# Kernel optimization log

Measured on AMD Instinct MI355X. Metric: run time of the kernel, lower is better.

The kernel has to match this reference:

```python
import jax, jax.numpy as jnp
import numpy as np
import math


def setup_inputs() -> dict:
    B, L, D, P, V = 4, 4096, 512, 128, 8
    key = jax.random.key(0)
    ki = iter(jax.random.split(key, 40))
    def rn(shape, s=0.02):
        return jax.random.normal(next(ki), shape, jnp.float32) * s
    z = lambda *s: jnp.zeros(s, jnp.float32)
    return dict(
        x=jax.random.normal(next(ki), (B, L, D), jnp.float32),
        W_omega=rn((D, D)), b_omega=z(D),
        omega_scale=jnp.full((D,), 0.01, jnp.float32),
        W_pi1=rn((D, D)), b_pi1=z(D), W_pi2=rn((D, D)), b_pi2=z(D),
        W_m1v=rn((D, D)), b_m1v=z(D),
        W_m1o=rn((D, D)), b_m1o=z(D),
        W_mag=rn((D, D)), b_mag=z(D),
        mag_scale=jnp.asarray(5.0, jnp.float32),
        W_qoff=rn((D, D)), b_qoff=z(D),
        W_kenc=rn((D, P)), b_kenc=z(P),
        W_venc=rn((D, V)), b_venc=z(V),
        W_sk1=rn((2 * D, D)), b_sk1=z(D),
        W_sk2=rn((D, P)), b_sk2=z(P),
        W_sg=rn((D, 1)), b_sg=z(1),
        W_kvo=rn((V, D)), b_kvo=z(D),
        ln_g=jnp.ones((4 * D,), jnp.float32), ln_b=z(4 * D),
        W_o1=rn((4 * D, 2 * D)), b_o1=z(2 * D),
        W_o2=rn((2 * D, D)), b_o2=z(D),
    )


def _lin(h, W, b):
    return h @ W + b


def _gelu(h):
    return jax.nn.gelu(h, approximate=False)  # torch nn.GELU default (erf)


def _forward(x, W_omega, b_omega, omega_scale, W_pi1, b_pi1, W_pi2, b_pi2,
             W_m1v, b_m1v, W_m1o, b_m1o, W_mag, b_mag, mag_scale,
             W_qoff, b_qoff, W_kenc, b_kenc, W_venc, b_venc,
             W_sk1, b_sk1, W_sk2, b_sk2, W_sg, b_sg, W_kvo, b_kvo,
             ln_g, ln_b, W_o1, b_o1, W_o2, b_o2):
    B, L, D = x.shape
    P = W_kenc.shape[1]
    # --- evolving phases ---
    omega_scaled = _lin(x, W_omega, b_omega) * jnp.abs(omega_scale)
    phi_init = _lin(_gelu(_lin(x, W_pi1, b_pi1)), W_pi2, b_pi2)
    phi = phi_init + jnp.cumsum(omega_scaled, axis=1)
    cos_phi, sin_phi = jnp.cos(phi), jnp.sin(phi)
    # --- memory 1: positional phasor memory ---
    v1 = _lin(x, W_m1v, b_m1v)
    magnitude = jax.nn.sigmoid(_lin(x, W_mag, b_mag)) * jnp.abs(mag_scale)
    wv1 = magnitude * v1
    sqrt_mag = jnp.sqrt(jnp.cumsum(magnitude, axis=1) + 1e-8)
    mem1_cos = jnp.cumsum(wv1 * cos_phi, axis=1) / sqrt_mag
    mem1_sin = jnp.cumsum(wv1 * sin_phi, axis=1) / sqrt_mag
    phi_q = phi + _lin(x, W_qoff, b_qoff)
    pos_ret = (mem1_cos * jnp.cos(phi_q) + mem1_sin * jnp.sin(phi_q)) / math.sqrt(D)
    pos_out = _lin(pos_ret, W_m1o, b_m1o)
    # --- memory 2: key/value phasor binding ---
    query_phase = jnp.tanh(_lin(x, W_kenc, b_kenc)) * math.pi
    values = _lin(x, W_venc, b_venc)                      # [B,L,V]
    store_gate = jax.nn.sigmoid(_lin(x, W_sg, b_sg))      # [B,L,1]
    positions = jnp.arange(1, L + 1, dtype=x.dtype)[None, :, None]
    context_avg = jnp.cumsum(x, axis=1) / positions
    sk_in = jnp.concatenate([x, context_avg], axis=-1)
    storage_phase = jnp.tanh(_lin(_gelu(_lin(sk_in, W_sk1, b_sk1)), W_sk2, b_sk2)) * math.pi
    store_cos, store_sin = jnp.cos(storage_phase), jnp.sin(storage_phase)  # [B,L,P]
    gv = values * store_gate                               # [B,L,V]
    # [B,L,P,V] outer products, cumsum along L
    kv_mem_cos = jnp.cumsum(store_cos[..., None] * gv[:, :, None, :], axis=1)
    kv_mem_sin = jnp.cumsum(store_sin[..., None] * gv[:, :, None, :], axis=1)
    gate_cum = jnp.clip(jnp.cumsum(store_gate, axis=1), 1.0, None)  # [B,L,1]
    inv_norm = (1.0 / jnp.sqrt(gate_cum))[..., None]
    kv_mem_cos = kv_mem_cos * inv_norm
    kv_mem_sin = kv_mem_sin * inv_norm
    q_cos, q_sin = jnp.cos(query_phase), jnp.sin(query_phase)
    kv_retrieved = (jnp.einsum('blp,blpv->blv', q_cos, kv_mem_cos)
                    + jnp.einsum('blp,blpv->blv', q_sin, kv_mem_sin)) / math.sqrt(P)
    kv_out = _lin(kv_retrieved, W_kvo, b_kvo)
    # --- output projection ---
    combined = jnp.concatenate([pos_out, kv_out, x * cos_phi, x * sin_phi], axis=-1)
    mu = combined.mean(axis=-1, keepdims=True)
    var = combined.var(axis=-1, keepdims=True)
    h = (combined - mu) / jnp.sqrt(var + 1e-5) * ln_g + ln_b
    h = _gelu(_lin(h, W_o1, b_o1))  # dropout is identity in eval mode
    return x + _lin(h, W_o2, b_o2)


def reference(x, W_omega, b_omega, omega_scale, W_pi1, b_pi1, W_pi2, b_pi2,
              W_m1v, b_m1v, W_m1o, b_m1o, W_mag, b_mag, mag_scale,
              W_qoff, b_qoff, W_kenc, b_kenc, W_venc, b_venc,
              W_sk1, b_sk1, W_sk2, b_sk2, W_sg, b_sg, W_kvo, b_kvo,
              ln_g, ln_b, W_o1, b_o1, W_o2, b_o2):
    return _forward(x, W_omega, b_omega, omega_scale, W_pi1, b_pi1, W_pi2, b_pi2,
                    W_m1v, b_m1v, W_m1o, b_m1o, W_mag, b_mag, mag_scale,
                    W_qoff, b_qoff, W_kenc, b_kenc, W_venc, b_venc,
                    W_sk1, b_sk1, W_sk2, b_sk2, W_sg, b_sg, W_kvo, b_kvo,
                    ln_g, ln_b, W_o1, b_o1, W_o2, b_o2)
```

## Files before the change

### kernel.cpp

```cpp
#include <hip/hip_runtime.h>
#include <math.h>

#define B_ 4
#define L_ 4096
#define D_ 512
#define P_ 128
#define V_ 8
#define N_ (B_*L_)
#define NC 64
#define CL (L_/NC)
#define LD ((size_t)L_*D_)
#define PI_F 3.14159265358979323846f

typedef unsigned short ushort;
typedef __attribute__((ext_vector_type(8))) short bh8;
typedef __attribute__((ext_vector_type(4))) float f4;
typedef const __attribute__((address_space(1))) unsigned int gu32;
typedef __attribute__((address_space(3))) unsigned int lu32;

__device__ __forceinline__ float geluf(float v){
    return 0.5f*v*(1.0f+erff(v*0.7071067811865475f));
}
__device__ __forceinline__ float tanhf_fast(float x){
    return 1.0f - 2.0f/(__expf(2.0f*x)+1.0f);
}
__device__ __forceinline__ ushort f2b(float f){
    union { float f; unsigned u; } v; v.f = f;
    unsigned r = (v.u + 0x7fffu + ((v.u >> 16) & 1u)) >> 16;
    return (ushort)r;
}
__device__ __forceinline__ float b2f(ushort h){
    union { unsigned u; float f; } v; v.u = ((unsigned)h) << 16;
    return v.f;
}
__device__ __forceinline__ void gload16(const ushort* g, ushort* l){
    __builtin_amdgcn_global_load_lds((gu32*)g, (lu32*)l, 16, 0, 0);
}
__device__ __forceinline__ int xcd_swz(int orig, int nwg){
    int q8 = nwg >> 3, r8 = nwg & 7;
    int xcd = orig & 7, sub = orig >> 3;
    return (xcd < r8 ? xcd*(q8+1) : r8*(q8+1) + (xcd-r8)*q8) + sub;
}

template<int ACT>
__global__ __launch_bounds__(512, 1)
void cgemm_k(const ushort* __restrict__ A, int lda,
             const ushort* __restrict__ Wt, const float* __restrict__ bias,
             ushort* __restrict__ Ob, float* __restrict__ Of,
             int ldc, int K, const float* __restrict__ addbuf)
{
    __shared__ ushort lA[2][256*64];
    __shared__ ushort lB[2][128*64];
    const int tid = threadIdx.x, lane = tid & 63, w = tid >> 6;
    const int wr = w >> 1, wc = w & 1;
    const int nbx = gridDim.x;
    const int wg = xcd_swz(blockIdx.y*nbx + blockIdx.x, nbx*gridDim.y);
    const int row0 = (wg / nbx) * 256, col0 = (wg % nbx) * 128;

    const int sr = tid >> 3, scp = tid & 7;
    const int scsrc = (scp ^ (sr & 7)) * 8;
    const ushort* gA = A  + (size_t)(row0 + sr) * lda + scsrc;
    const ushort* gB = Wt + (size_t)(col0 + sr) * K   + scsrc;
    const int dof = sr*64 + scp*8;

    f4 zero4 = {0.f,0.f,0.f,0.f};
    f4 acc[4][4];
    #pragma unroll
    for (int i=0;i<4;i++)
        #pragma unroll
        for (int j=0;j<4;j++) acc[i][j] = zero4;

    auto stage = [&](int buf, int kt){
        #pragma unroll
        for (int is=0; is<4; ++is)
            gload16(gA + (size_t)is*64*lda + kt, &lA[buf][is*64*64 + dof]);
        #pragma unroll
        for (int is=0; is<2; ++is)
            gload16(gB + (size_t)is*64*K + kt, &lB[buf][is*64*64 + dof]);
    };

    const int NT = K >> 6;
    stage(0, 0);
    for (int t2=0; t2<NT; ++t2){
        int cur = t2 & 1;
        if (t2+1 < NT){
            stage(cur^1, (t2+1)<<6);
            asm volatile("s_waitcnt vmcnt(6)" ::: "memory");
        } else {
            asm volatile("s_waitcnt vmcnt(0)" ::: "memory");
        }
        __builtin_amdgcn_s_barrier();
        __builtin_amdgcn_sched_barrier(0);
        #pragma unroll
        for (int h=0; h<2; ++h){
            bh8 af[4], bf_[4];
            #pragma unroll
            for (int i=0;i<4;i++){
                int row = wr*64 + i*16 + (lane & 15);
                int pc = (h*4 + (lane >> 4)) ^ (row & 7);
                af[i] = *(const bh8*)&lA[cur][row*64 + pc*8];
            }
            #pragma unroll
            for (int j=0;j<4;j++){
                int row = wc*64 + j*16 + (lane & 15);
                int pc = (h*4 + (lane >> 4)) ^ (row & 7);
                bf_[j] = *(const bh8*)&lB[cur][row*64 + pc*8];
            }
            #pragma unroll
            for (int i=0;i<4;i++)
                #pragma unroll
                for (int j=0;j<4;j++)
                    acc[i][j] = __builtin_amdgcn_mfma_f32_16x16x32_bf16(af[i], bf_[j], acc[i][j], 0, 0, 0);
        }
        __builtin_amdgcn_sched_barrier(0);
        __builtin_amdgcn_s_barrier();
    }

    #pragma unroll
    for (int i=0;i<4;i++){
        int rr = row0 + wr*64 + i*16 + ((lane >> 4) << 2);
        #pragma unroll
        for (int j=0;j<4;j++){
            int cc = col0 + wc*64 + j*16 + (lane & 15);
            float bv = bias[cc];
            #pragma unroll
            for (int q=0;q<4;q++){
                int r = rr + q;
                float t = acc[i][j][q] + bv;
                if (ACT==2){
                    if (addbuf) t += addbuf[(size_t)r*512 + cc];
                    Of[(size_t)r*ldc + cc] = t;
                } else {
                    if (ACT==1) t = geluf(t);
                    Ob[(size_t)r*ldc + cc] = f2b(t);
                }
            }
        }
    }
}

__global__ __launch_bounds__(256, 2)
void fgemm_k(const ushort* __restrict__ A, int lda, const ushort* __restrict__ Wt,
             const float* __restrict__ bs0, const float* __restrict__ bs1,
             const float* __restrict__ bs2, const float* __restrict__ bs3,
             const float* __restrict__ bs4, const float* __restrict__ bs5,
             ushort* __restrict__ o0, ushort* __restrict__ o1p, ushort* __restrict__ o2p,
             ushort* __restrict__ o3p, ushort* __restrict__ o4p,
             ushort* __restrict__ Qc, ushort* __restrict__ Qs,
             const float* __restrict__ omsc, const float* __restrict__ magscp, int K)
{
    __shared__ ushort lA[2][128*32];
    __shared__ ushort lB[2][128*32];
    const int tid = threadIdx.x, lane = tid & 63, w = tid >> 6;
    const int wr = w >> 1, wc = w & 1;
    const int nbx = gridDim.x;
    const int wg = xcd_swz(blockIdx.y*nbx + blockIdx.x, nbx*gridDim.y);
    const int row0 = (wg / nbx) * 128, col0 = (wg % nbx) * 128;

    const int srow = w*32 + (lane >> 2);
    const int scol = (lane & 3) * 8;
    const ushort* gA0 = A  + (size_t)(row0 + srow)      * lda + scol;
    const ushort* gA1 = A  + (size_t)(row0 + srow + 16) * lda + scol;
    const ushort* gB0 = Wt + (size_t)(col0 + srow)      * K   + scol;
    const ushort* gB1 = Wt + (size_t)(col0 + srow + 16) * K   + scol;
    const int d0 = srow*32 + scol, d1 = (srow+16)*32 + scol;

    f4 zero4 = {0.f,0.f,0.f,0.f};
    f4 acc[4][4];
    #pragma unroll
    for (int i=0;i<4;i++)
        #pragma unroll
        for (int j=0;j<4;j++) acc[i][j] = zero4;

    const int fr = lane & 15, fq = (lane >> 4) * 8;
    gload16(gA0, &lA[0][d0]); gload16(gA1, &lA[0][d1]);
    gload16(gB0, &lB[0][d0]); gload16(gB1, &lB[0][d1]);
    __syncthreads();
    int cur = 0;
    for (int kt = 0; kt < K; kt += 32) {
        int nxt = cur ^ 1;
        if (kt + 32 < K) {
            gload16(gA0 + kt + 32, &lA[nxt][d0]); gload16(gA1 + kt + 32, &lA[nxt][d1]);
            gload16(gB0 + kt + 32, &lB[nxt][d0]); gload16(gB1 + kt + 32, &lB[nxt][d1]);
        }
        bh8 af[4], bfr[4];
        #pragma unroll
        for (int i=0;i<4;i++){
            af[i]  = *(const bh8*)&lA[cur][(wr*64 + i*16 + fr)*32 + fq];
            bfr[i] = *(const bh8*)&lB[cur][(wc*64 + i*16 + fr)*32 + fq];
        }
        #pragma unroll
        for (int i=0;i<4;i++)
            #pragma unroll
            for (int j=0;j<4;j++)
                acc[i][j] = __builtin_amdgcn_mfma_f32_16x16x32_bf16(af[i], bfr[j], acc[i][j], 0, 0, 0);
        __syncthreads();
        cur = nxt;
    }

    const int seg = col0 >> 9;
    if (seg == 5) {
        #pragma unroll
        for (int i=0;i<4;i++){
            int rr = row0 + wr*64 + i*16 + ((lane >> 4) << 2);
            #pragma unroll
            for (int j=0;j<4;j++){
                int lcc = (col0 - 2560) + wc*64 + j*16 + (lane & 15);
                float bv = bs5[lcc];
                #pragma unroll
                for (int q=0;q<4;q++){
                    int r = rr + q;
                    float ph = tanhf_fast(acc[i][j][q] + bv)*PI_F;
                    Qc[(size_t)r*128 + lcc] = f2b(__cosf(ph));
                    Qs[(size_t)r*128 + lcc] = f2b(__sinf(ph));
                }
            }
        }
        return;
    }
    const float* bias = seg==0?bs0: seg==1?bs1: seg==2?bs2: seg==3?bs3: bs4;
    ushort* dst = seg==0?o0: seg==1?o1p: seg==2?o2p: seg==3?o3p: o4p;
    float msc = fabsf(*magscp);
    #pragma unroll
    for (int i=0;i<4;i++){
        int rr = row0 + wr*64 + i*16 + ((lane >> 4) << 2);
        #pragma unroll
        for (int j=0;j<4;j++){
            int cc = col0 + wc*64 + j*16 + (lane & 15);
            int lcc = cc & 511;
            float bv = bias[lcc];
            float csc = (seg==0) ? fabsf(omsc[lcc]) : 1.0f;
            #pragma unroll
            for (int q=0;q<4;q++){
                int r = rr + q;
                float t = acc[i][j][q] + bv;
                if (seg==1)      t = msc/(1.0f+__expf(-t));
                else if (seg==3) t = geluf(t);
                else             t *= csc;
                dst[(size_t)r*512 + lcc] = f2b(t);
            }
        }
    }
}

__global__ __launch_bounds__(256, 2)
void mgemm_k(const ushort* __restrict__ Apos, const ushort* __restrict__ Ask,
             const ushort* __restrict__ Wm1o, const ushort* __restrict__ Wsk2,
             const float* __restrict__ bm1o, const float* __restrict__ bsk2,
             ushort* __restrict__ planes, ushort* __restrict__ Kc, ushort* __restrict__ Ks)
{
    __shared__ ushort lA[2][128*32];
    __shared__ ushort lB[2][128*32];
    const int tid = threadIdx.x, lane = tid & 63, w = tid >> 6;
    const int wr = w >> 1, wc = w & 1;
    const int nbx = gridDim.x;
    const int wg = xcd_swz(blockIdx.y*nbx + blockIdx.x, nbx*gridDim.y);
    const int row0 = (wg / nbx) * 128, col0 = (wg % nbx) * 128;
    const int seg = col0 >> 9;
    const ushort* A  = seg ? Ask  : Apos;
    const ushort* Wt = seg ? Wsk2 : Wm1o;
    const int wcol0 = seg ? (col0 - 512) : col0;
    const int K = 512;

    const int srow = w*32 + (lane >> 2);
    const int scol = (lane & 3) * 8;
    const ushort* gA0 = A  + (size_t)(row0 + srow)       * 512 + scol;
    const ushort* gA1 = A  + (size_t)(row0 + srow + 16)  * 512 + scol;
    const ushort* gB0 = Wt + (size_t)(wcol0 + srow)      * 512 + scol;
    const ushort* gB1 = Wt + (size_t)(wcol0 + srow + 16) * 512 + scol;
    const int d0 = srow*32 + scol, d1 = (srow+16)*32 + scol;

    f4 zero4 = {0.f,0.f,0.f,0.f};
    f4 acc[4][4];
    #pragma unroll
    for (int i=0;i<4;i++)
        #pragma unroll
        for (int j=0;j<4;j++) acc[i][j] = zero4;

    const int fr = lane & 15, fq = (lane >> 4) * 8;
    gload16(gA0, &lA[0][d0]); gload16(gA1, &lA[0][d1]);
    gload16(gB0, &lB[0][d0]); gload16(gB1, &lB[0][d1]);
    __syncthreads();
    int cur = 0;
    for (int kt = 0; kt < K; kt += 32) {
        int nxt = cur ^ 1;
        if (kt + 32 < K) {
            gload16(gA0 + kt + 32, &lA[nxt][d0]); gload16(gA1 + kt + 32, &lA[nxt][d1]);
            gload16(gB0 + kt + 32, &lB[nxt][d0]); gload16(gB1 + kt + 32, &lB[nxt][d1]);
        }
        bh8 af[4], bfr[4];
        #pragma unroll
        for (int i=0;i<4;i++){
            af[i]  = *(const bh8*)&lA[cur][(wr*64 + i*16 + fr)*32 + fq];
            bfr[i] = *(const bh8*)&lB[cur][(wc*64 + i*16 + fr)*32 + fq];
        }
        #pragma unroll
        for (int i=0;i<4;i++)
            #pragma unroll
            for (int j=0;j<4;j++)
                acc[i][j] = __builtin_amdgcn_mfma_f32_16x16x32_bf16(af[i], bfr[j], acc[i][j], 0, 0, 0);
        __syncthreads();
        cur = nxt;
    }

    #pragma unroll
    for (int i=0;i<4;i++){
        int rr = row0 + wr*64 + i*16 + ((lane >> 4) << 2);
        #pragma unroll
        for (int j=0;j<4;j++){
            int cc = col0 + wc*64 + j*16 + (lane & 15);
            #pragma unroll
            for (int q=0;q<4;q++){
                int r = rr + q;
                if (seg == 0){
                    planes[(size_t)r*2048 + cc] = f2b(acc[i][j][q] + bm1o[cc]);
                } else {
                    int lcc = cc - 512;
                    float ph = tanhf_fast(acc[i][j][q] + bsk2[lcc])*PI_F;
                    Kc[(size_t)r*128 + lcc] = f2b(__cosf(ph));
                    Ks[(size_t)r*128 + lcc] = f2b(__sinf(ph));
                }
            }
        }
    }
}

__global__ __launch_bounds__(256)
void wtrans_k(const float* __restrict__ W, ushort* __restrict__ Wt, int K, int M)
{
    __shared__ float tile[32][33];
    int kb = blockIdx.y*32, mb = blockIdx.x*32;
    int tx = threadIdx.x & 31, ty = threadIdx.x >> 5;
    #pragma unroll
    for (int i = ty; i < 32; i += 8)
        tile[i][tx] = W[(size_t)(kb+i)*M + mb+tx];
    __syncthreads();
    #pragma unroll
    for (int i = ty; i < 32; i += 8)
        Wt[(size_t)(mb+i)*K + kb+tx] = f2b(tile[tx][i]);
}

__global__ __launch_bounds__(256)
void fconv_k(const float* __restrict__ in, ushort* __restrict__ xctx)
{
    size_t i = ((size_t)blockIdx.x*256 + threadIdx.x) * 4;
    size_t row = i >> 9; int d = (int)(i & 511);
    float4 v = *(const float4*)(in + i);
    ushort* o = xctx + row*1024 + d;
    o[0]=f2b(v.x); o[1]=f2b(v.y); o[2]=f2b(v.z); o[3]=f2b(v.w);
}

__global__ __launch_bounds__(256)
void s1a_k(const ushort* __restrict__ omega, const float* __restrict__ xg,
           float* __restrict__ csA, float* __restrict__ csX)
{
    int bid = blockIdx.x;
    int b = bid >> 7; int rem = bid & 127;
    int dg = rem & 1, c = rem >> 1;
    int d = dg*256 + threadIdx.x;
    size_t base = ((size_t)b*L_ + (size_t)c*CL)*D_ + d;
    float sA=0.f, sX=0.f;
    for (int l=0;l<CL;l++){
        sA += b2f(omega[base + (size_t)l*D_]);
        sX += xg[base + (size_t)l*D_];
    }
    size_t ci = ((size_t)b*NC + c)*D_ + d;
    csA[ci]=sA; csX[ci]=sX;
}

__global__ __launch_bounds__(256)
void aux1_k(float* __restrict__ csA, float* __restrict__ csX,
            const float* __restrict__ sgate, float* __restrict__ rinv, int nb2)
{
    __shared__ float wsum[4];
    __shared__ float carry;
    int bb = blockIdx.x, t = threadIdx.x;
    if (bb < nb2){
        int tt = bb*256 + t;
        int b = tt >> 9, d = tt & 511;
        float* bufs[2] = {csA, csX};
        #pragma unroll
        for (int i=0;i<2;i++){
            float* p = bufs[i] + ((size_t)b*NC)*D_ + d;
            float run=0.f;
            for (int c=0;c<NC;c++){
                float v = p[(size_t)c*D_];
                p[(size_t)c*D_] = run;
                run += v;
            }
        }
        return;
    }
    int b = bb - nb2;
    int lane = t & 63, wave = t >> 6;
    if (t == 0) carry = 0.f;
    __syncthreads();
    for (int s = 0; s < L_/256; s++){
        float v = sgate[(size_t)b*L_ + s*256 + t];
        float sc = v;
        #pragma unroll
        for (int off=1; off<64; off<<=1){
            float u = __shfl_up(sc, off, 64);
            if (lane >= off) sc += u;
        }
        if (lane == 63) wsum[wave] = sc;
        __syncthreads();
        float woff = carry;
        for (int w2 = 0; w2 < wave; w2++) woff += wsum[w2];
        float inc = sc + woff;
        rinv[(size_t)b*L_ + s*256 + t] = rsqrtf(fmaxf(inc, 1.0f));
        __syncthreads();
        if (t == 255) carry = inc;
        __syncthreads();
    }
}

__global__ void prefix_k(float* a, float* b2v, float* c3, int nbuf)
{
    int t = blockIdx.x*blockDim.x + threadIdx.x;
    int b = t >> 9, d = t & 511;
    float* bufs[3] = {a,b2v,c3};
    for (int i=0;i<nbuf;i++){
        float* p = bufs[i] + ((size_t)b*NC)*D_ + d;
        float run=0.f;
        for (int c=0;c<NC;c++){
            float v = p[(size_t)c*D_];
            p[(size_t)c*D_] = run;
            run += v;
        }
    }
}

__global__ __launch_bounds__(256)
void s1c_k(const ushort* __restrict__ omega, const float* __restrict__ xg,
           const ushort* __restrict__ phi_init,
           const ushort* __restrict__ magn, const ushort* __restrict__ v1,
           const float* __restrict__ csA, const float* __restrict__ csX,
           ushort* __restrict__ cphi, ushort* __restrict__ sphi, ushort* __restrict__ xctx,
           float* __restrict__ csM, float* __restrict__ csC, float* __restrict__ csS)
{
    int bid = blockIdx.x;
    int b = bid >> 7; int rem = bid & 127;
    int dg = rem & 1, c = rem >> 1;
    int d = dg*256 + threadIdx.x;
    size_t ci = ((size_t)b*NC + c)*D_ + d;
    float phiacc = csA[ci], xacc = csX[ci];
    float sM=0.f,sC=0.f,sS=0.f;
    size_t xrow = (size_t)b*L_ + (size_t)c*CL;
    size_t base = xrow*D_ + d;
    for (int l=0;l<CL;l++){
        size_t idx = base + (size_t)l*D_;
        phiacc += b2f(omega[idx]);
        float ph = b2f(phi_init[idx]) + phiacc;
        float spv = __sinf(ph), cpv = __cosf(ph);
        cphi[idx] = f2b(cpv); sphi[idx] = f2b(spv);
        xacc += xg[idx];
        xctx[(xrow + l)*1024 + 512 + d] = f2b(__fdividef(xacc, (float)(c*CL + l + 1)));
        float m = b2f(magn[idx]); sM += m;
        float wv = m * b2f(v1[idx]);
        sC = fmaf(wv, cpv, sC); sS = fmaf(wv, spv, sS);
    }
    csM[ci]=sM; csC[ci]=sC; csS[ci]=sS;
}

__global__ __launch_bounds__(256)
void s1e_k(const ushort* __restrict__ magn, const ushort* __restrict__ v1,
           const ushort* qoff, const ushort* __restrict__ cphi, const ushort* __restrict__ sphi,
           const float* __restrict__ csM, const float* __restrict__ csC,
           const float* __restrict__ csS, ushort* pos_ret)
{
    int bid = blockIdx.x;
    int b = bid >> 7; int rem = bid & 127;
    int dg = rem & 1, c = rem >> 1;
    int d = dg*256 + threadIdx.x;
    size_t ci = ((size_t)b*NC + c)*D_ + d;
    float mA=csM[ci], cA=csC[ci], sA=csS[ci];
    size_t base = ((size_t)b*L_ + (size_t)c*CL)*D_ + d;
    for (int l=0;l<CL;l++){
        size_t idx = base + (size_t)l*D_;
        float m = b2f(magn[idx]); mA += m;
        float wv = m * b2f(v1[idx]);
        float cp = b2f(cphi[idx]), sp = b2f(sphi[idx]);
        cA = fmaf(wv, cp, cA); sA = fmaf(wv, sp, sA);
        float rs = rsqrtf(mA + 1e-8f);
        float qo = b2f(qoff[idx]);
        float sq = __sinf(qo), cq = __cosf(qo);
        float cosq = cp*cq - sp*sq;
        float sinq = sp*cq + cp*sq;
        pos_ret[idx] = f2b((cA*cosq + sA*sinq) * rs * 0.04419417382415922f);
    }
}

__global__ __launch_bounds__(256)
void vencsg_k(const float* __restrict__ xg, const float* __restrict__ Wv,
              const float* __restrict__ bv, const float* __restrict__ Wg,
              const float* __restrict__ bg,
              ushort* __restrict__ gvb, float* __restrict__ sgate)
{
    int gw = (int)((blockIdx.x*(size_t)blockDim.x + threadIdx.x) >> 6);
    int lane = threadIdx.x & 63;
    const float* xr = xg + (size_t)gw*D_;
    float pv[8] = {0,0,0,0,0,0,0,0}; float pg = 0.f;
    #pragma unroll
    for (int j=0;j<8;j++){
        int k = lane + 64*j;
        float xv = xr[k];
        #pragma unroll
        for (int v=0;v<8;v++) pv[v] = fmaf(xv, Wv[k*8+v], pv[v]);
        pg = fmaf(xv, Wg[k], pg);
    }
    #pragma unroll
    for (int off=32; off>0; off>>=1){
        #pragma unroll
        for (int v=0;v<8;v++) pv[v] += __shfl_down(pv[v], off, 64);
        pg += __shfl_down(pg, off, 64);
    }
    if (lane==0){
        float sg = 1.0f/(1.0f+__expf(-(pg + bg[0])));
        #pragma unroll
        for (int v=0;v<8;v++) gvb[(size_t)gw*8+v] = f2b((pv[v] + bv[v]) * sg);
        sgate[gw] = sg;
    }
}

__global__ __launch_bounds__(256)
void kvsum_k(const ushort* __restrict__ Kc, const ushort* __restrict__ Ks,
             const ushort* __restrict__ gvb, float* __restrict__ csKV)
{
    int bid = blockIdx.x;
    int b = bid >> 6, c = bid & 63;
    int t = threadIdx.x; int p = t & 127; int v0 = (t>>7)*4;
    size_t row0 = (size_t)b*L_ + (size_t)c*64;
    float ac[4]={0,0,0,0}, as[4]={0,0,0,0};
    for (int l=0;l<64;l++){
        size_t r = row0 + l;
        float kc = b2f(Kc[r*(size_t)P_ + p]);
        float ks = b2f(Ks[r*(size_t)P_ + p]);
        #pragma unroll
        for (int j=0;j<4;j++){
            float gv = b2f(gvb[r*(size_t)V_ + v0 + j]);
            ac[j] = fmaf(kc, gv, ac[j]);
            as[j] = fmaf(ks, gv, as[j]);
        }
    }
    float* base = csKV + ((size_t)b*64 + c)*2048;
    #pragma unroll
    for (int j=0;j<4;j++){
        base[p*V_ + v0 + j] = ac[j];
        base[1024 + p*V_ + v0 + j] = as[j];
    }
}

__global__ void kvpfx_k(float* __restrict__ csKV)
{
    int t = blockIdx.x*blockDim.x + threadIdx.x;
    int b = t >> 11, si = t & 2047;
    float* ptr = csKV + ((size_t)b*64)*2048 + si;
    float run=0.f;
    for (int c=0;c<64;c++){
        float v = ptr[(size_t)c*2048];
        ptr[(size_t)c*2048] = run;
        run += v;
    }
}

__global__ __launch_bounds__(256)
void kv2_k(const ushort* __restrict__ Qc, const ushort* __restrict__ Qs,
           const ushort* __restrict__ Kc, const ushort* __restrict__ Ks,
           const ushort* __restrict__ gvb, const float* __restrict__ rinv,
           const float* __restrict__ csKV, float* __restrict__ kvret)
{
    __shared__ ushort sS[64][66];
    __shared__ float sM[2048];
    __shared__ float sgv[64][8];
    int tile = blockIdx.x, b = blockIdx.y;
    int t = threadIdx.x, lane = t & 63, w = t >> 6;
    int wr = w >> 1, wc = w & 1;
    size_t row0 = (size_t)b*L_ + (size_t)tile*64;
    const float* kvb = csKV + ((size_t)b*64 + tile)*2048;
    #pragma unroll
    for (int k=0;k<8;k++) sM[t + k*256] = kvb[t + k*256];
    #pragma unroll
    for (int k=0;k<2;k++){
        int idx = t + k*256; int l = idx >> 3, v = idx & 7;
        sgv[l][v] = b2f(gvb[(row0 + l)*(size_t)V_ + v]);
    }
    f4 zero4 = {0.f,0.f,0.f,0.f};
    f4 acc[2][2];
    #pragma unroll
    for (int i=0;i<2;i++)
        #pragma unroll
        for (int j=0;j<2;j++) acc[i][j] = zero4;
    #pragma unroll
    for (int ks=0; ks<8; ks++){
        const ushort* Ab = (ks<4) ? Qc : Qs;
        const ushort* Bb = (ks<4) ? Kc : Ks;
        int kb = (ks&3)*32 + (lane>>4)*8;
        bh8 af[2], bfr[2];
        #pragma unroll
        for (int i=0;i<2;i++)
            af[i] = *(const bh8*)(Ab + (row0 + wr*32 + i*16 + (lane&15))*(size_t)P_ + kb);
        #pragma unroll
        for (int j=0;j<2;j++)
            bfr[j] = *(const bh8*)(Bb + (row0 + wc*32 + j*16 + (lane&15))*(size_t)P_ + kb);
        #pragma unroll
        for (int i=0;i<2;i++)
            #pragma unroll
            for (int j=0;j<2;j++)
                acc[i][j] = __builtin_amdgcn_mfma_f32_16x16x32_bf16(af[i], bfr[j], acc[i][j], 0, 0, 0);
    }
    #pragma unroll
    for (int i=0;i<2;i++){
        #pragma unroll
        for (int j=0;j<2;j++){
            int cc = wc*32 + j*16 + (lane & 15);
            #pragma unroll
            for (int q=0;q<4;q++){
                int lr = wr*32 + i*16 + ((lane>>4)<<2) + q;
                sS[lr][cc] = f2b((cc <= lr) ? acc[i][j][q] : 0.f);
            }
        }
    }
    __syncthreads();
    int l = t & 63, vh = t >> 6; int v0 = vh*2;
    const ushort* qcr = Qc + (row0 + l)*(size_t)P_;
    const ushort* qsr = Qs + (row0 + l)*(size_t)P_;
    float a0=0.f, a1=0.f;
    #pragma unroll
    for (int pc=0; pc<16; pc++){
        bh8 qc8 = *(const bh8*)(qcr + pc*8);
        bh8 qs8 = *(const bh8*)(qsr + pc*8);
        #pragma unroll
        for (int e=0;e<8;e++){
            int p = pc*8+e;
            float qc = b2f((ushort)qc8[e]), qs = b2f((ushort)qs8[e]);
            a0 += qc*sM[p*8+v0]   + qs*sM[1024+p*8+v0];
            a1 += qc*sM[p*8+v0+1] + qs*sM[1024+p*8+v0+1];
        }
    }
    for (int c=0;c<64;c++){
        float sv = b2f(sS[l][c]);
        a0 = fmaf(sv, sgv[c][v0],   a0);
        a1 = fmaf(sv, sgv[c][v0+1], a1);
    }
    float rn = rinv[row0 + l] * 0.08838834764831845f;
    kvret[(row0+l)*(size_t)V_ + v0]   = a0*rn;
    kvret[(row0+l)*(size_t)V_ + v0+1] = a1*rn;
}

__global__ __launch_bounds__(256)
void kvo_k(const float* __restrict__ kvret, const float* __restrict__ Wkvo,
           const float* __restrict__ bkvo, ushort* __restrict__ pl)
{
    size_t idx = (size_t)blockIdx.x*256 + threadIdx.x;
    size_t n = idx >> 9; int d = (int)(idx & 511);
    float s = bkvo[d];
    #pragma unroll
    for (int v=0;v<8;v++) s = fmaf(kvret[n*8+v], Wkvo[v*512 + d], s);
    pl[n*2048 + 512 + d] = f2b(s);
}

__global__ __launch_bounds__(256)
void cmb_k(const float* __restrict__ xg, const ushort* __restrict__ cphi,
           const ushort* __restrict__ sphi,
           const float* __restrict__ ln_g, const float* __restrict__ ln_b,
           ushort* pl)
{
    __shared__ float red[8];
    int n = blockIdx.x; int t = threadIdx.x;
    int wave = t>>6, lane = t&63;
    float v_[8]; float sum=0.f, sumsq=0.f;
    #pragma unroll
    for (int i=0;i<8;i++){
        int cidx = t + i*256;
        int seg = cidx >> 9, cc = cidx & 511;
        float v;
        if (seg <= 1) v = b2f(pl[(size_t)n*2048 + cidx]);
        else {
            size_t id = (size_t)n*D_ + cc;
            v = xg[id] * b2f((seg==2) ? cphi[id] : sphi[id]);
        }
        v_[i]=v; sum += v; sumsq = fmaf(v,v,sumsq);
    }
    #pragma unroll
    for (int off=32; off>0; off>>=1){
        sum += __shfl_xor(sum, off, 64);
        sumsq += __shfl_xor(sumsq, off, 64);
    }
    if (lane==0){ red[wave]=sum; red[wave+4]=sumsq; }
    __syncthreads();
    float s = red[0]+red[1]+red[2]+red[3];
    float q = red[4]+red[5]+red[6]+red[7];
    float mu = s * (1.0f/2048.0f);
    float var = q * (1.0f/2048.0f) - mu*mu;
    float rstd = rsqrtf(var + 1e-5f);
    #pragma unroll
    for (int i=0;i<8;i++){
        int cidx = t + i*256;
        float h = (v_[i]-mu)*rstd*ln_g[cidx] + ln_b[cidx];
        pl[(size_t)n*2048 + cidx] = f2b(h);
    }
}

__global__ void copyx_k(const float* __restrict__ x, float* __restrict__ out, size_t n)
{
    size_t i = (size_t)blockIdx.x*256 + threadIdx.x;
    if (i < n) out[i] = x[i];
}

struct WS {
    ushort *wt_fused,*wt_pi2,*wt_sk1,*wt_sk2,*wt_m1o,*wt_o1,*wt_o2;
    ushort *xctx, *pool;
    ushort *Qc,*Qs,*Kc,*Ks,*gvb,*cphi,*sphi;
    float *sgate,*rinv,*kvret;
    float *csA,*csX,*csM,*csC,*csS,*csKV;
};

static size_t ws_layout(WS& w, char* base, int NB)
{
    size_t off = 0;
    auto al = [&](size_t bytes)->char* {
        char* p = base + off; off = (off + bytes + 255) & ~(size_t)255; return p;
    };
    size_t R = (size_t)NB * L_;
    w.wt_fused=(ushort*)al((size_t)2688*512*2);
    w.wt_pi2 =(ushort*)al(512*512*2);
    w.wt_sk1 =(ushort*)al((size_t)512*1024*2); w.wt_sk2=(ushort*)al(128*512*2);
    w.wt_m1o =(ushort*)al(512*512*2);
    w.wt_o1  =(ushort*)al((size_t)1024*2048*2); w.wt_o2=(ushort*)al((size_t)512*1024*2);
    w.xctx=(ushort*)al(R*1024*2);
    w.pool=(ushort*)al(R*512*2*6);
    w.Qc=(ushort*)al(R*128*2); w.Qs=(ushort*)al(R*128*2);
    w.Kc=(ushort*)al(R*128*2); w.Ks=(ushort*)al(R*128*2);
    w.gvb=(ushort*)al(R*8*2);
    w.cphi=(ushort*)al(R*512*2); w.sphi=(ushort*)al(R*512*2);
    w.sgate=(float*)al(R*4); w.rinv=(float*)al(R*4); w.kvret=(float*)al(R*8*4);
    w.csA=(float*)al((size_t)NB*NC*512*4); w.csX=(float*)al((size_t)NB*NC*512*4);
    w.csM=(float*)al((size_t)NB*NC*512*4); w.csC=(float*)al((size_t)NB*NC*512*4);
    w.csS=(float*)al((size_t)NB*NC*512*4);
    w.csKV=(float*)al((size_t)NB*64*2048*4);
    return off;
}

extern "C" void kernel_launch(void* const* d_in, const int* in_sizes, int n_in,
                              void* d_out, int out_size, void* d_ws, size_t ws_size,
                              hipStream_t stream)
{
    const float* x        =(const float*)d_in[0];
    const float* W_omega  =(const float*)d_in[1];  const float* b_omega=(const float*)d_in[2];
    const float* omega_sc =(const float*)d_in[3];
    const float* W_pi1    =(const float*)d_in[4];  const float* b_pi1 =(const float*)d_in[5];
    const float* W_pi2    =(const float*)d_in[6];  const float* b_pi2 =(const float*)d_in[7];
    const float* W_m1v    =(const float*)d_in[8];  const float* b_m1v =(const float*)d_in[9];
    const float* W_m1o    =(const float*)d_in[10]; const float* b_m1o =(const float*)d_in[11];
    const float* W_mag    =(const float*)d_in[12]; const float* b_mag =(const float*)d_in[13];
    const float* mag_sc   =(const float*)d_in[14];
    const float* W_qoff   =(const float*)d_in[15]; const float* b_qoff=(const float*)d_in[16];
    const float* W_kenc   =(const float*)d_in[17]; const float* b_kenc=(const float*)d_in[18];
    const float* W_venc   =(const float*)d_in[19]; const float* b_venc=(const float*)d_in[20];
    const float* W_sk1    =(const float*)d_in[21]; const float* b_sk1 =(const float*)d_in[22];
    const float* W_sk2    =(const float*)d_in[23]; const float* b_sk2 =(const float*)d_in[24];
    const float* W_sg     =(const float*)d_in[25]; const float* b_sg  =(const float*)d_in[26];
    const float* W_kvo    =(const float*)d_in[27]; const float* b_kvo =(const float*)d_in[28];
    const float* ln_g     =(const float*)d_in[29]; const float* ln_b  =(const float*)d_in[30];
    const float* W_o1     =(const float*)d_in[31]; const float* b_o1  =(const float*)d_in[32];
    const float* W_o2     =(const float*)d_in[33]; const float* b_o2  =(const float*)d_in[34];
    float* out = (float*)d_out;

    char* wsb = (char*)d_ws;
    WS w;
    int NB = 4;
    if (ws_layout(w, wsb, 4) > ws_size) {
        NB = 2;
        if (ws_layout(w, wsb, 2) > ws_size) {
            NB = 1;
            if (ws_layout(w, wsb, 1) > ws_size) {
                copyx_k<<<dim3((unsigned)(((size_t)N_*D_ + 255)/256)), dim3(256), 0, stream>>>(x, out, (size_t)N_*D_);
                return;
            }
        }
    }

    dim3 blk(256);
    auto wt = [&](const float* W, ushort* Wt, int K, int M){
        wtrans_k<<<dim3(M/32, K/32), blk, 0, stream>>>(W, Wt, K, M);
    };
    wt(W_omega, w.wt_fused + (size_t)0*512*512, 512, 512);
    wt(W_mag,   w.wt_fused + (size_t)1*512*512, 512, 512);
    wt(W_m1v,   w.wt_fused + (size_t)2*512*512, 512, 512);
    wt(W_pi1,   w.wt_fused + (size_t)3*512*512, 512, 512);
    wt(W_qoff,  w.wt_fused + (size_t)4*512*512, 512, 512);
    wt(W_kenc,  w.wt_fused + (size_t)5*512*512, 512, 128);
    wt(W_pi2,w.wt_pi2,512,512);
    wt(W_sk1,w.wt_sk1,1024,512);  wt(W_sk2,w.wt_sk2,512,128);
    wt(W_m1o,w.wt_m1o,512,512);
    wt(W_o1,w.wt_o1,2048,1024);   wt(W_o2,w.wt_o2,1024,512);

    const int R = NB * L_;
    const size_t SL = (size_t)R * 512;
    ushort* bA = w.pool;        ushort* bB = w.pool + SL;
    ushort* bC = w.pool + 2*SL; ushort* bD = w.pool + 3*SL;
    ushort* bE = w.pool + 4*SL; ushort* bF = w.pool + 5*SL;
    ushort* planes = w.pool;
    ushort* h1 = w.pool + 4*SL;

    #define CGEMM(ACT,A,lda,Wt_,bias_,Ob_,Of_,ldc,K_,M_,add_) \
        cgemm_k<ACT><<<dim3((M_)/128, R/256), dim3(512), 0, stream>>>(A,lda,Wt_,bias_,Ob_,Of_,ldc,K_,add_)

    for (int g = 0; g < B_/NB; ++g) {
        const float* xg = x + (size_t)g*NB*LD;
        float* outg = out + (size_t)g*NB*LD;

        fconv_k<<<dim3((unsigned)((size_t)R*512/1024)), blk, 0, stream>>>(xg, w.xctx);

        fgemm_k<<<dim3(2688/128, R/128), blk, 0, stream>>>(
            w.xctx,1024, w.wt_fused, b_omega,b_mag,b_m1v,b_pi1,b_qoff,b_kenc,
            bA,bB,bC,bD,bF, w.Qc,w.Qs, omega_sc, mag_sc, 512);
        CGEMM(0, bD,512, w.wt_pi2, b_pi2, bE,(float*)0, 512, 512,512, (const float*)0);
        vencsg_k<<<dim3((unsigned)((size_t)R*64/256)), blk, 0, stream>>>(xg, W_venc,b_venc, W_sg,b_sg, w.gvb, w.sgate);
        s1a_k<<<dim3(NB*NC*2), blk, 0, stream>>>(bA, xg, w.csA, w.csX);
        aux1_k<<<dim3(NB*2 + NB), blk, 0, stream>>>(w.csA, w.csX, w.sgate, w.rinv, NB*2);
        s1c_k<<<dim3(NB*NC*2), blk, 0, stream>>>(bA, xg, bE, bB, bC, w.csA, w.csX,
                                                 w.cphi, w.sphi, w.xctx, w.csM, w.csC, w.csS);
        prefix_k<<<dim3(NB*2), blk, 0, stream>>>(w.csM, w.csC, w.csS, 3);
        s1e_k<<<dim3(NB*NC*2), blk, 0, stream>>>(bB, bC, bF, w.cphi, w.sphi,
                                                 w.csM, w.csC, w.csS, bF);

        CGEMM(1, w.xctx,1024, w.wt_sk1, b_sk1, bD,(float*)0, 512, 1024,512, (const float*)0);
        mgemm_k<<<dim3(640/128, R/128), blk, 0, stream>>>(
            bF, bD, w.wt_m1o, w.wt_sk2, b_m1o, b_sk2, planes, w.Kc, w.Ks);

        kvsum_k<<<dim3(NB*64), blk, 0, stream>>>(w.Kc, w.Ks, w.gvb, w.csKV);
        kvpfx_k<<<dim3(NB*8), blk, 0, stream>>>(w.csKV);
        kv2_k<<<dim3(64, NB), blk, 0, stream>>>(w.Qc, w.Qs, w.Kc, w.Ks, w.gvb, w.rinv, w.csKV, w.kvret);
        kvo_k<<<dim3((unsigned)((size_t)R*512/256)), blk, 0, stream>>>(w.kvret, W_kvo, b_kvo, planes);

        cmb_k<<<dim3(R), blk, 0, stream>>>(xg, w.cphi, w.sphi, ln_g, ln_b, planes);
        CGEMM(1, planes,2048, w.wt_o1, b_o1, h1,(float*)0, 1024, 2048,1024, (const float*)0);
        CGEMM(2, h1,1024, w.wt_o2, b_o2, (ushort*)0,outg, 512, 1024,512, xg);
    }
    #undef CGEMM
}
```

Baseline: 546.4 us.

## Shrink GEMM tiles to 128x128, batch weight transposes, fuse kvo into LayerNorm

The main bf16 GEMM moves from 256x128 tiles with 512 threads and one block per CU to 128x128 tiles with 256 threads and two blocks per CU. This doubles the grid and gives more occupancy for latency hiding, at the cost of less operand reuse per tile. The twelve weight-transpose launches are merged into one kernel that looks up which matrix each block handles. The small kv output projection is folded into the combine/LayerNorm kernel, which removes a launch and a round trip of that plane through memory.

```diff
diff --git a/kernel.cpp b/kernel.cpp
--- a/kernel.cpp
+++ b/kernel.cpp
@@ -43,25 +43,19 @@
 }
 
 template<int ACT>
-__global__ __launch_bounds__(512, 1)
-void cgemm_k(const ushort* __restrict__ A, int lda,
+__global__ __launch_bounds__(256, 2)
+void dgemm_k(const ushort* __restrict__ A, int lda,
              const ushort* __restrict__ Wt, const float* __restrict__ bias,
              ushort* __restrict__ Ob, float* __restrict__ Of,
              int ldc, int K, const float* __restrict__ addbuf)
 {
-    __shared__ ushort lA[2][256*64];
+    __shared__ ushort lA[2][128*64];
     __shared__ ushort lB[2][128*64];
     const int tid = threadIdx.x, lane = tid & 63, w = tid >> 6;
     const int wr = w >> 1, wc = w & 1;
     const int nbx = gridDim.x;
     const int wg = xcd_swz(blockIdx.y*nbx + blockIdx.x, nbx*gridDim.y);
-    const int row0 = (wg / nbx) * 256, col0 = (wg % nbx) * 128;
-
-    const int sr = tid >> 3, scp = tid & 7;
-    const int scsrc = (scp ^ (sr & 7)) * 8;
-    const ushort* gA = A  + (size_t)(row0 + sr) * lda + scsrc;
-    const ushort* gB = Wt + (size_t)(col0 + sr) * K   + scsrc;
-    const int dof = sr*64 + scp*8;
+    const int row0 = (wg / nbx) * 128, col0 = (wg % nbx) * 128;
 
     f4 zero4 = {0.f,0.f,0.f,0.f};
     f4 acc[4][4];
@@ -72,20 +66,28 @@
 
     auto stage = [&](int buf, int kt){
         #pragma unroll
-        for (int is=0; is<4; ++is)
-            gload16(gA + (size_t)is*64*lda + kt, &lA[buf][is*64*64 + dof]);
-        #pragma unroll
-        for (int is=0; is<2; ++is)
-            gload16(gB + (size_t)is*64*K + kt, &lB[buf][is*64*64 + dof]);
+        for (int is=0; is<4; ++is){
+            int id = tid + is*256;
+            int r = id >> 3, p = id & 7;
+            int srcc = (p ^ (r & 7)) * 8;
+            gload16(A + (size_t)(row0 + r)*lda + kt + srcc, &lA[buf][r*64 + p*8]);
+        }
+        #pragma unroll
+        for (int is=0; is<4; ++is){
+            int id = tid + is*256;
+            int r = id >> 3, p = id & 7;
+            int srcc = (p ^ (r & 7)) * 8;
+            gload16(Wt + (size_t)(col0 + r)*K + kt + srcc, &lB[buf][r*64 + p*8]);
+        }
     };
 
     const int NT = K >> 6;
     stage(0, 0);
-    for (int t2=0; t2<NT; ++t2){
+    for (int t2 = 0; t2 < NT; ++t2){
         int cur = t2 & 1;
-        if (t2+1 < NT){
-            stage(cur^1, (t2+1)<<6);
-            asm volatile("s_waitcnt vmcnt(6)" ::: "memory");
+        if (t2 + 1 < NT){
+            stage(cur ^ 1, (t2+1) << 6);
+            asm volatile("s_waitcnt vmcnt(8)" ::: "memory");
         } else {
             asm volatile("s_waitcnt vmcnt(0)" ::: "memory");
         }
@@ -325,11 +327,23 @@
     }
 }
 
-__global__ __launch_bounds__(256)
-void wtrans_k(const float* __restrict__ W, ushort* __restrict__ Wt, int K, int M)
+struct WtArgs {
+    const float* src[12];
+    ushort* dst[12];
+    int K[12], M[12], t0[13];
+};
+__global__ __launch_bounds__(256)
+void wtall_k(WtArgs a)
 {
     __shared__ float tile[32][33];
-    int kb = blockIdx.y*32, mb = blockIdx.x*32;
+    int bb = blockIdx.x;
+    int j = 0;
+    while (bb >= a.t0[j+1]) ++j;
+    int tt = bb - a.t0[j];
+    int K = a.K[j], M = a.M[j];
+    int mt = M >> 5;
+    int kb = (tt / mt) * 32, mb = (tt % mt) * 32;
+    const float* W = a.src[j]; ushort* Wt = a.dst[j];
     int tx = threadIdx.x & 31, ty = threadIdx.x >> 5;
     #pragma unroll
     for (int i = ty; i < 32; i += 8)
@@ -649,34 +663,31 @@
 }
 
 __global__ __launch_bounds__(256)
-void kvo_k(const float* __restrict__ kvret, const float* __restrict__ Wkvo,
-           const float* __restrict__ bkvo, ushort* __restrict__ pl)
-{
-    size_t idx = (size_t)blockIdx.x*256 + threadIdx.x;
-    size_t n = idx >> 9; int d = (int)(idx & 511);
-    float s = bkvo[d];
-    #pragma unroll
-    for (int v=0;v<8;v++) s = fmaf(kvret[n*8+v], Wkvo[v*512 + d], s);
-    pl[n*2048 + 512 + d] = f2b(s);
-}
-
-__global__ __launch_bounds__(256)
 void cmb_k(const float* __restrict__ xg, const ushort* __restrict__ cphi,
            const ushort* __restrict__ sphi,
+           const float* __restrict__ kvret, const float* __restrict__ Wkvo,
+           const float* __restrict__ bkvo,
            const float* __restrict__ ln_g, const float* __restrict__ ln_b,
            ushort* pl)
 {
     __shared__ float red[8];
+    __shared__ float kvv[8];
     int n = blockIdx.x; int t = threadIdx.x;
     int wave = t>>6, lane = t&63;
+    if (t < 8) kvv[t] = kvret[(size_t)n*8 + t];
+    __syncthreads();
     float v_[8]; float sum=0.f, sumsq=0.f;
     #pragma unroll
     for (int i=0;i<8;i++){
         int cidx = t + i*256;
         int seg = cidx >> 9, cc = cidx & 511;
         float v;
-        if (seg <= 1) v = b2f(pl[(size_t)n*2048 + cidx]);
-        else {
+        if (seg == 0) v = b2f(pl[(size_t)n*2048 + cidx]);
+        else if (seg == 1) {
+            v = bkvo[cc];
+            #pragma unroll
+            for (int vv=0; vv<8; vv++) v = fmaf(kvv[vv], Wkvo[vv*512 + cc], v);
+        } else {
             size_t id = (size_t)n*D_ + cc;
             v = xg[id] * b2f((seg==2) ? cphi[id] : sphi[id]);
         }
@@ -782,19 +793,22 @@
     }
 
     dim3 blk(256);
-    auto wt = [&](const float* W, ushort* Wt, int K, int M){
-        wtrans_k<<<dim3(M/32, K/32), blk, 0, stream>>>(W, Wt, K, M);
-    };
-    wt(W_omega, w.wt_fused + (size_t)0*512*512, 512, 512);
-    wt(W_mag,   w.wt_fused + (size_t)1*512*512, 512, 512);
-    wt(W_m1v,   w.wt_fused + (size_t)2*512*512, 512, 512);
-    wt(W_pi1,   w.wt_fused + (size_t)3*512*512, 512, 512);
-    wt(W_qoff,  w.wt_fused + (size_t)4*512*512, 512, 512);
-    wt(W_kenc,  w.wt_fused + (size_t)5*512*512, 512, 128);
-    wt(W_pi2,w.wt_pi2,512,512);
-    wt(W_sk1,w.wt_sk1,1024,512);  wt(W_sk2,w.wt_sk2,512,128);
-    wt(W_m1o,w.wt_m1o,512,512);
-    wt(W_o1,w.wt_o1,2048,1024);   wt(W_o2,w.wt_o2,1024,512);
+    WtArgs wa;
+    const float* srcs[12] = {W_omega, W_mag, W_m1v, W_pi1, W_qoff, W_kenc,
+                             W_pi2, W_sk1, W_sk2, W_m1o, W_o1, W_o2};
+    ushort* dsts[12] = {w.wt_fused + (size_t)0*512*512, w.wt_fused + (size_t)1*512*512,
+                        w.wt_fused + (size_t)2*512*512, w.wt_fused + (size_t)3*512*512,
+                        w.wt_fused + (size_t)4*512*512, w.wt_fused + (size_t)5*512*512,
+                        w.wt_pi2, w.wt_sk1, w.wt_sk2, w.wt_m1o, w.wt_o1, w.wt_o2};
+    int Ks_[12] = {512,512,512,512,512,512, 512,1024,512,512,2048,1024};
+    int Ms_[12] = {512,512,512,512,512,128, 512, 512,128,512,1024, 512};
+    int cum = 0;
+    for (int j = 0; j < 12; ++j){
+        wa.src[j]=srcs[j]; wa.dst[j]=dsts[j]; wa.K[j]=Ks_[j]; wa.M[j]=Ms_[j];
+        wa.t0[j]=cum; cum += (Ks_[j]/32)*(Ms_[j]/32);
+    }
+    wa.t0[12]=cum;
+    wtall_k<<<dim3(cum), blk, 0, stream>>>(wa);
 
     const int R = NB * L_;
     const size_t SL = (size_t)R * 512;
@@ -804,8 +818,8 @@
     ushort* planes = w.pool;
     ushort* h1 = w.pool + 4*SL;
 
-    #define CGEMM(ACT,A,lda,Wt_,bias_,Ob_,Of_,ldc,K_,M_,add_) \
-        cgemm_k<ACT><<<dim3((M_)/128, R/256), dim3(512), 0, stream>>>(A,lda,Wt_,bias_,Ob_,Of_,ldc,K_,add_)
+    #define DGEMM(ACT,A,lda,Wt_,bias_,Ob_,Of_,ldc,K_,M_,add_) \
+        dgemm_k<ACT><<<dim3((M_)/128, R/128), blk, 0, stream>>>(A,lda,Wt_,bias_,Ob_,Of_,ldc,K_,add_)
 
     for (int g = 0; g < B_/NB; ++g) {
         const float* xg = x + (size_t)g*NB*LD;
@@ -816,7 +830,7 @@
         fgemm_k<<<dim3(2688/128, R/128), blk, 0, stream>>>(
             w.xctx,1024, w.wt_fused, b_omega,b_mag,b_m1v,b_pi1,b_qoff,b_kenc,
             bA,bB,bC,bD,bF, w.Qc,w.Qs, omega_sc, mag_sc, 512);
-        CGEMM(0, bD,512, w.wt_pi2, b_pi2, bE,(float*)0, 512, 512,512, (const float*)0);
+        DGEMM(0, bD,512, w.wt_pi2, b_pi2, bE,(float*)0, 512, 512,512, (const float*)0);
         vencsg_k<<<dim3((unsigned)((size_t)R*64/256)), blk, 0, stream>>>(xg, W_venc,b_venc, W_sg,b_sg, w.gvb, w.sgate);
         s1a_k<<<dim3(NB*NC*2), blk, 0, stream>>>(bA, xg, w.csA, w.csX);
         aux1_k<<<dim3(NB*2 + NB), blk, 0, stream>>>(w.csA, w.csX, w.sgate, w.rinv, NB*2);
@@ -826,18 +840,18 @@
         s1e_k<<<dim3(NB*NC*2), blk, 0, stream>>>(bB, bC, bF, w.cphi, w.sphi,
                                                  w.csM, w.csC, w.csS, bF);
 
-        CGEMM(1, w.xctx,1024, w.wt_sk1, b_sk1, bD,(float*)0, 512, 1024,512, (const float*)0);
+        DGEMM(1, w.xctx,1024, w.wt_sk1, b_sk1, bD,(float*)0, 512, 1024,512, (const float*)0);
         mgemm_k<<<dim3(640/128, R/128), blk, 0, stream>>>(
             bF, bD, w.wt_m1o, w.wt_sk2, b_m1o, b_sk2, planes, w.Kc, w.Ks);
 
         kvsum_k<<<dim3(NB*64), blk, 0, stream>>>(w.Kc, w.Ks, w.gvb, w.csKV);
         kvpfx_k<<<dim3(NB*8), blk, 0, stream>>>(w.csKV);
         kv2_k<<<dim3(64, NB), blk, 0, stream>>>(w.Qc, w.Qs, w.Kc, w.Ks, w.gvb, w.rinv, w.csKV, w.kvret);
-        kvo_k<<<dim3((unsigned)((size_t)R*512/256)), blk, 0, stream>>>(w.kvret, W_kvo, b_kvo, planes);
-
-        cmb_k<<<dim3(R), blk, 0, stream>>>(xg, w.cphi, w.sphi, ln_g, ln_b, planes);
-        CGEMM(1, planes,2048, w.wt_o1, b_o1, h1,(float*)0, 1024, 2048,1024, (const float*)0);
-        CGEMM(2, h1,1024, w.wt_o2, b_o2, (ushort*)0,outg, 512, 1024,512, xg);
-    }
-    #undef CGEMM
-}
+
+        cmb_k<<<dim3(R), blk, 0, stream>>>(xg, w.cphi, w.sphi, w.kvret, W_kvo, b_kvo,
+                                           ln_g, ln_b, planes);
+        DGEMM(1, planes,2048, w.wt_o1, b_o1, h1,(float*)0, 1024, 2048,1024, (const float*)0);
+        DGEMM(2, h1,1024, w.wt_o2, b_o2, (ushort*)0,outg, 512, 1024,512, xg);
+    }
+    #undef DGEMM
+}
```

New measurement: 477.6 us. 1.14x faster.
